# Performance work log

Measured on AMD Instinct MI355X. Metric: run time of the kernel, lower is better.

Reference implementation:

```python
import jax, jax.numpy as jnp
import numpy as np

KX = jnp.array([[-1., 0., 1.], [-2., 0., 2.], [-1., 0., 1.]], dtype=jnp.float32).reshape(1, 1, 3, 3)
KY = jnp.array([[1., 2., 1.], [0., 0., 0.], [-1., -2., -1.]], dtype=jnp.float32).reshape(1, 1, 3, 3)

def _sobel(x, k):
    # x: [B,1,H,W], k: [1,1,3,3]; stride 1, padding 1 -> same spatial size
    return jax.lax.conv_general_dilated(
        x, k, window_strides=(1, 1), padding=((1, 1), (1, 1)),
        dimension_numbers=('NCHW', 'OIHW', 'NCHW'))

def setup_inputs() -> dict:
    key = jax.random.key(0)
    k1, k2 = jax.random.split(key)
    B, C, H, W = 32, 1, 512, 512
    output = jax.random.normal(k1, (B, C, H, W), dtype=jnp.float32)
    target = jax.random.normal(k2, (B, C, H, W), dtype=jnp.float32)
    return {"output": output, "target": target}

def reference(output, target):
    gx_t = _sobel(target, KX)
    gy_t = _sobel(target, KY)
    gx_o = _sobel(output, KX)
    gy_o = _sobel(output, KY)
    grad_loss = jnp.mean((gx_t - gx_o) ** 2) + jnp.mean((gy_t - gy_o) ** 2)
    return grad_loss
```

## Files before the change

kernel.cpp:

```cpp
#include <hip/hip_runtime.h>


#define BATCH 32
#define HH 512
#define WW 512
#define RROWS 16
#define TPB 256
#define LSTRIDE (WW + 8)
#define NPART (BATCH * (HH / RROWS))

__global__ __launch_bounds__(TPB) void sobel_partial_kernel(
    const float* __restrict__ out_img,
    const float* __restrict__ tgt_img,
    float* __restrict__ partials)
{
    __shared__ float lds[(RROWS + 2) * LSTRIDE];
    __shared__ float wsum[TPB / 64];

    const int tid = threadIdx.x;
    const int bid = blockIdx.x;
    const int tilesPerImg = HH / RROWS;
    const int b  = bid / tilesPerImg;
    const int y0 = (bid % tilesPerImg) * RROWS;
    const size_t imgBase = (size_t)b * HH * WW;

    if (tid < RROWS + 2) {
        lds[tid * LSTRIDE + 3]      = 0.f;
        lds[tid * LSTRIDE + WW + 4] = 0.f;
    }

    #pragma unroll
    for (int i = tid; i < (RROWS + 2) * (WW / 4); i += TPB) {
        const int r  = i >> 7;
        const int c4 = i & 127;
        const int g  = y0 - 1 + r;
        const int c  = c4 * 4;
        float4 d4;
        if ((unsigned)g < (unsigned)HH) {
            const float4 o = *(const float4*)(out_img + imgBase + (size_t)g * WW + c);
            const float4 t = *(const float4*)(tgt_img + imgBase + (size_t)g * WW + c);
            d4 = make_float4(t.x - o.x, t.y - o.y, t.z - o.z, t.w - o.w);
        } else {
            d4 = make_float4(0.f, 0.f, 0.f, 0.f);
        }
        *(float4*)(lds + r * LSTRIDE + 4 + c) = d4;
    }
    __syncthreads();

    float acc = 0.f;
    #pragma unroll
    for (int cc = 0; cc < WW / TPB; ++cc) {
        const int xi = 4 + cc * TPB + tid;
        const float* p = lds + xi;
        float a0 = p[-1],            b0 = p[0],            c0 = p[1];
        float a1 = p[LSTRIDE - 1],   b1 = p[LSTRIDE],      c1 = p[LSTRIDE + 1];
        #pragma unroll
        for (int r = 0; r < RROWS; ++r) {
            const float* q = p + (r + 2) * LSTRIDE;
            const float a2 = q[-1];
            const float b2 = q[0];
            const float c2 = q[1];
            const float gx = (c0 - a0) + 2.f * (c1 - a1) + (c2 - a2);
            const float gy = (a0 + 2.f * b0 + c0) - (a2 + 2.f * b2 + c2);
            acc = fmaf(gx, gx, acc);
            acc = fmaf(gy, gy, acc);
            a0 = a1; b0 = b1; c0 = c1;
            a1 = a2; b1 = b2; c1 = c2;
        }
    }

    #pragma unroll
    for (int off = 32; off > 0; off >>= 1)
        acc += __shfl_down(acc, off, 64);
    const int wid = tid >> 6;
    if ((tid & 63) == 0) wsum[wid] = acc;
    __syncthreads();
    if (tid == 0)
        partials[bid] = wsum[0] + wsum[1] + wsum[2] + wsum[3];
}

__global__ __launch_bounds__(TPB) void reduce_partials_kernel(
    const float* __restrict__ partials, float* __restrict__ out)
{
    const int tid = threadIdx.x;
    float s = 0.f;
    #pragma unroll
    for (int i = 0; i < NPART / TPB; ++i)
        s += partials[tid + i * TPB];
    #pragma unroll
    for (int off = 32; off > 0; off >>= 1)
        s += __shfl_down(s, off, 64);
    __shared__ float w[TPB / 64];
    if ((tid & 63) == 0) w[tid >> 6] = s;
    __syncthreads();
    if (tid == 0)
        out[0] = (w[0] + w[1] + w[2] + w[3]) * (1.0f / ((float)BATCH * HH * WW));
}

extern "C" void kernel_launch(void* const* d_in, const int* in_sizes, int n_in,
                              void* d_out, int out_size, void* d_ws, size_t ws_size,
                              hipStream_t stream) {
    (void)in_sizes; (void)n_in; (void)ws_size; (void)out_size;
    const float* out_img = (const float*)d_in[0];
    const float* tgt_img = (const float*)d_in[1];
    float* partials = (float*)d_ws;
    float* res = (float*)d_out;

    sobel_partial_kernel<<<NPART, TPB, 0, stream>>>(out_img, tgt_img, partials);
    reduce_partials_kernel<<<1, TPB, 0, stream>>>(partials, res);
}
```

Baseline: 20.49 us.

## Replace LDS tile with per-wave register stencil using cross-lane shuffles

Each wavefront now handles one full 512-wide strip of 16 rows. It keeps the horizontal Sobel partials in a 3-row register ring buffer and gets neighbour columns through lane shuffles instead of a shared-memory tile, which removes the LDS staging, the block-level barrier and the shared-memory reads. The separable form (horizontal smooth/diff, then vertical combine) cuts arithmetic per pixel. In exchange, register pressure rises, there are more shuffles per row, and load latency is no longer hidden by a block-wide bulk load.

Result: faster. 19.84 us (-3.2%).

```diff
diff --git a/kernel.cpp b/kernel.cpp
--- a/kernel.cpp
+++ b/kernel.cpp
@@ -4,79 +4,89 @@
 #define BATCH 32
 #define HH 512
 #define WW 512
-#define RROWS 16
+#define RW 16
 #define TPB 256
-#define LSTRIDE (WW + 8)
-#define NPART (BATCH * (HH / RROWS))
+#define NPART (BATCH * (HH / RW))
 
 __global__ __launch_bounds__(TPB) void sobel_partial_kernel(
     const float* __restrict__ out_img,
     const float* __restrict__ tgt_img,
     float* __restrict__ partials)
 {
-    __shared__ float lds[(RROWS + 2) * LSTRIDE];
-    __shared__ float wsum[TPB / 64];
+    const int tid  = threadIdx.x;
+    const int lane = tid & 63;
+    const int w    = blockIdx.x * (TPB / 64) + (tid >> 6);
+    const int img  = w >> 5;
+    const int y0   = (w & 31) * RW;
 
-    const int tid = threadIdx.x;
-    const int bid = blockIdx.x;
-    const int tilesPerImg = HH / RROWS;
-    const int b  = bid / tilesPerImg;
-    const int y0 = (bid % tilesPerImg) * RROWS;
-    const size_t imgBase = (size_t)b * HH * WW;
+    const size_t base = (size_t)img * HH * WW;
+    const float* ob = out_img + base;
+    const float* tb = tgt_img + base;
+    const int x1 = lane * 4;
+    const int x2 = 256 + lane * 4;
 
-    if (tid < RROWS + 2) {
-        lds[tid * LSTRIDE + 3]      = 0.f;
-        lds[tid * LSTRIDE + WW + 4] = 0.f;
-    }
+    float hs[3][8];
+    float hd[3][8];
+    float acc = 0.f;
 
     #pragma unroll
-    for (int i = tid; i < (RROWS + 2) * (WW / 4); i += TPB) {
-        const int r  = i >> 7;
-        const int c4 = i & 127;
-        const int g  = y0 - 1 + r;
-        const int c  = c4 * 4;
-        float4 d4;
+    for (int i = 0; i < RW + 2; ++i) {
+        const int g   = y0 - 1 + i;
+        const int cur = i % 3;
+
+        float4 d1, d2;
         if ((unsigned)g < (unsigned)HH) {
-            const float4 o = *(const float4*)(out_img + imgBase + (size_t)g * WW + c);
-            const float4 t = *(const float4*)(tgt_img + imgBase + (size_t)g * WW + c);
-            d4 = make_float4(t.x - o.x, t.y - o.y, t.z - o.z, t.w - o.w);
+            const float* orow = ob + (size_t)g * WW;
+            const float* trow = tb + (size_t)g * WW;
+            const float4 o1 = *(const float4*)(orow + x1);
+            const float4 t1 = *(const float4*)(trow + x1);
+            const float4 o2 = *(const float4*)(orow + x2);
+            const float4 t2 = *(const float4*)(trow + x2);
+            d1 = make_float4(t1.x - o1.x, t1.y - o1.y, t1.z - o1.z, t1.w - o1.w);
+            d2 = make_float4(t2.x - o2.x, t2.y - o2.y, t2.z - o2.z, t2.w - o2.w);
         } else {
-            d4 = make_float4(0.f, 0.f, 0.f, 0.f);
+            d1 = make_float4(0.f, 0.f, 0.f, 0.f);
+            d2 = make_float4(0.f, 0.f, 0.f, 0.f);
         }
-        *(float4*)(lds + r * LSTRIDE + 4 + c) = d4;
-    }
-    __syncthreads();
 
-    float acc = 0.f;
-    #pragma unroll
-    for (int cc = 0; cc < WW / TPB; ++cc) {
-        const int xi = 4 + cc * TPB + tid;
-        const float* p = lds + xi;
-        float a0 = p[-1],            b0 = p[0],            c0 = p[1];
-        float a1 = p[LSTRIDE - 1],   b1 = p[LSTRIDE],      c1 = p[LSTRIDE + 1];
-        #pragma unroll
-        for (int r = 0; r < RROWS; ++r) {
-            const float* q = p + (r + 2) * LSTRIDE;
-            const float a2 = q[-1];
-            const float b2 = q[0];
-            const float c2 = q[1];
-            const float gx = (c0 - a0) + 2.f * (c1 - a1) + (c2 - a2);
-            const float gy = (a0 + 2.f * b0 + c0) - (a2 + 2.f * b2 + c2);
-            acc = fmaf(gx, gx, acc);
-            acc = fmaf(gy, gy, acc);
-            a0 = a1; b0 = b1; c0 = c1;
-            a1 = a2; b1 = b2; c1 = c2;
+        float dl1 = __shfl_up(d1.w, 1, 64);
+        if (lane == 0) dl1 = 0.f;
+        const float s2x = __shfl(d2.x, 0, 64);
+        float dr1 = __shfl_down(d1.x, 1, 64);
+        if (lane == 63) dr1 = s2x;
+        const float s1w = __shfl(d1.w, 63, 64);
+        float dl2 = __shfl_up(d2.w, 1, 64);
+        if (lane == 0) dl2 = s1w;
+        float dr2 = __shfl_down(d2.x, 1, 64);
+        if (lane == 63) dr2 = 0.f;
+
+        hs[cur][0] = fmaf(2.f, d1.x, dl1 + d1.y);  hd[cur][0] = d1.y - dl1;
+        hs[cur][1] = fmaf(2.f, d1.y, d1.x + d1.z); hd[cur][1] = d1.z - d1.x;
+        hs[cur][2] = fmaf(2.f, d1.z, d1.y + d1.w); hd[cur][2] = d1.w - d1.y;
+        hs[cur][3] = fmaf(2.f, d1.w, d1.z + dr1);  hd[cur][3] = dr1 - d1.z;
+        hs[cur][4] = fmaf(2.f, d2.x, dl2 + d2.y);  hd[cur][4] = d2.y - dl2;
+        hs[cur][5] = fmaf(2.f, d2.y, d2.x + d2.z); hd[cur][5] = d2.z - d2.x;
+        hs[cur][6] = fmaf(2.f, d2.z, d2.y + d2.w); hd[cur][6] = d2.w - d2.y;
+        hs[cur][7] = fmaf(2.f, d2.w, d2.z + dr2);  hd[cur][7] = dr2 - d2.z;
+
+        if (i >= 2) {
+            const int top = (i - 2) % 3;
+            const int mid = (i - 1) % 3;
+            #pragma unroll
+            for (int j = 0; j < 8; ++j) {
+                const float gx = fmaf(2.f, hd[mid][j], hd[top][j] + hd[cur][j]);
+                const float gy = hs[top][j] - hs[cur][j];
+                acc = fmaf(gx, gx, acc);
+                acc = fmaf(gy, gy, acc);
+            }
         }
     }
 
     #pragma unroll
     for (int off = 32; off > 0; off >>= 1)
         acc += __shfl_down(acc, off, 64);
-    const int wid = tid >> 6;
-    if ((tid & 63) == 0) wsum[wid] = acc;
-    __syncthreads();
-    if (tid == 0)
-        partials[bid] = wsum[0] + wsum[1] + wsum[2] + wsum[3];
+    if (lane == 0)
+        partials[w] = acc;
 }
 
 __global__ __launch_bounds__(TPB) void reduce_partials_kernel(
@@ -90,11 +100,12 @@
     #pragma unroll
     for (int off = 32; off > 0; off >>= 1)
         s += __shfl_down(s, off, 64);
-    __shared__ float w[TPB / 64];
-    if ((tid & 63) == 0) w[tid >> 6] = s;
+    __shared__ float wsum[TPB / 64];
+    if ((tid & 63) == 0) wsum[tid >> 6] = s;
     __syncthreads();
     if (tid == 0)
-        out[0] = (w[0] + w[1] + w[2] + w[3]) * (1.0f / ((float)BATCH * HH * WW));
+        out[0] = (wsum[0] + wsum[1] + wsum[2] + wsum[3])
+               * (1.0f / ((float)BATCH * HH * WW));
 }
 
 extern "C" void kernel_launch(void* const* d_in, const int* in_sizes, int n_in,
@@ -106,6 +117,6 @@
     float* partials = (float*)d_ws;
     float* res = (float*)d_out;
 
-    sobel_partial_kernel<<<NPART, TPB, 0, stream>>>(out_img, tgt_img, partials);
+    sobel_partial_kernel<<<NPART / (TPB / 64), TPB, 0, stream>>>(out_img, tgt_img, partials);
     reduce_partials_kernel<<<1, TPB, 0, stream>>>(partials, res);
 }
```
